# Performance work log

Hardware: AMD Instinct MI355X
Metric: run time of the kernel (lower is better)

The kernel has to match this reference:

```python
import jax, jax.numpy as jnp
import numpy as np

K = 1  # BaseSnapFunction.k default

def setup_inputs() -> dict:
    key = jax.random.key(0)
    k1, k2 = jax.random.split(key)
    B, S, D = 4, 2048, 1024
    C, N = 16, 2048          # num_codebooks, num_codes
    x = jax.random.normal(k1, (B, S, D), dtype=jnp.float32)
    codebook = jax.random.normal(k2, (C, N, D // C), dtype=jnp.float32)
    return {"x": x, "codebook": codebook}

def reference(x, codebook):
    B, S, D = x.shape
    C, N, sub = codebook.shape
    xr = x.reshape(B, S, C, sub)                      # split dim into C chunks
    # squared euclidean distance (monotone in true distance -> same argmin)
    dots = jnp.einsum('bscd,cnd->bscn', xr, codebook)  # [B,S,C,N]
    xsq = jnp.sum(xr * xr, axis=-1)                    # [B,S,C]
    cbsq = jnp.sum(codebook * codebook, axis=-1)       # [C,N]
    d2 = xsq[..., None] - 2.0 * dots + cbsq[None, None]
    idx = jnp.argmin(d2, axis=-1)                      # [B,S,C], k=1 topk of -dist
    # gather per-codebook features and concat chunks back to dim
    quant = codebook[jnp.arange(C)[None, None, :], idx]  # [B,S,C,sub]
    out = quant.reshape(B, S, D) / K
    return out
```

## Files before the change

kernel.cpp:

```cpp
#include <hip/hip_runtime.h>

constexpr int BS    = 8192;
constexpr int CCH   = 16;
constexpr int NCODE = 2048;

using s16x8 = __attribute__((ext_vector_type(8))) short;
using f32x4 = __attribute__((ext_vector_type(4))) float;


__device__ __forceinline__ unsigned short bf16_rne(float v) {
    unsigned u = __float_as_uint(v);
    return (unsigned short)((u + 0x7fffu + ((u >> 16) & 1u)) >> 16);
}
__device__ __forceinline__ void split1(float v, unsigned short& h, unsigned short& l) {
    h = bf16_rne(v);
    const float hf = __uint_as_float((unsigned)h << 16);
    l = bf16_rne(v - hf);
}
__device__ __forceinline__ void split4(float4 v, ushort4& h, ushort4& l) {
    split1(v.x, h.x, l.x); split1(v.y, h.y, l.y);
    split1(v.z, h.z, l.z); split1(v.w, h.w, l.w);
}
__device__ __forceinline__ unsigned enc_f(float s) {
    unsigned u = __float_as_uint(s);
    return (u & 0x80000000u) ? ~u : (u | 0x80000000u);
}

__device__ __forceinline__ s16x8 ldfrag(const char* buf, int row, int ke) {
    return *(const s16x8*)(buf + row * 128 + ((((ke >> 3) ^ row) & 7) * 16));
}

__device__ __forceinline__ void gload16(const void* g, void* l) {
    __builtin_amdgcn_global_load_lds(
        (const __attribute__((address_space(1))) void*)g,
        (__attribute__((address_space(3))) void*)l, 16, 0, 0);
}

__global__ void cbsq_kernel(const float* __restrict__ cb, float* __restrict__ cbsq,
                            float* __restrict__ cmax)
{
    const int g = blockIdx.x * 256 + threadIdx.x;
    const float4* cg = (const float4*)cb;
    float s = 0.f;
#pragma unroll
    for (int q = 0; q < 16; ++q) {
        float4 v = cg[(size_t)g * 16 + q];
        s = fmaf(v.x, v.x, s); s = fmaf(v.y, v.y, s);
        s = fmaf(v.z, v.z, s); s = fmaf(v.w, v.w, s);
    }
    cbsq[g] = s;
    atomicMax((unsigned*)cmax, __float_as_uint(s));
}

__global__ void presplit_cb(const float* __restrict__ cb,
                            unsigned short* __restrict__ cbh,
                            unsigned short* __restrict__ cbl)
{
    const int g = blockIdx.x * 256 + threadIdx.x;
    const float4 v = ((const float4*)cb)[g];
    ushort4 h, l; split4(v, h, l);
    ((ushort4*)cbh)[g] = h;
    ((ushort4*)cbl)[g] = l;
}

__global__ __launch_bounds__(256, 2)
void vq_fp32_fallback(const float* __restrict__ x, const float* __restrict__ cb,
                      float* __restrict__ out)
{
    __shared__ __align__(16) char smraw[65536];
    float4 (*xs)[128] = reinterpret_cast<float4(*)[128]>(smraw);
    float4 (*cs)[128] = reinterpret_cast<float4(*)[128]>(smraw + 32768);
    float  (*rs)[128] = reinterpret_cast<float(*)[128]>(smraw);
    int    (*ri)[128] = reinterpret_cast<int(*)[128]>(smraw + 8192);
    int    *bfin      = reinterpret_cast<int*>(smraw + 16384);

    const int tid = threadIdx.x, tx = tid & 15, ty = tid >> 4;
    const int c = blockIdx.y, mbase = blockIdx.x * 128;
    const float4* xg = (const float4*)x;
    const float4* cg = (const float4*)cb;
    {
        const int k4 = tid & 15, mrow0 = tid >> 4;
#pragma unroll
        for (int i = 0; i < 8; ++i) {
            const int m = i * 16 + mrow0;
            xs[k4][m] = xg[(size_t)(mbase + m) * 256 + c * 16 + k4];
        }
    }
    float best[8]; int bidx[8];
#pragma unroll
    for (int ii = 0; ii < 8; ++ii) { best[ii] = 3.4e38f; bidx[ii] = 0; }
    for (int nt = 0; nt < 16; ++nt) {
        __syncthreads();
        {
            const int k4 = tid & 15, nrow0 = tid >> 4;
#pragma unroll
            for (int i = 0; i < 8; ++i) {
                const int n = i * 16 + nrow0;
                cs[k4][n] = cg[((size_t)c * NCODE + nt * 128 + n) * 16 + k4];
            }
        }
        __syncthreads();
        float acc[8][8], csq[8];
#pragma unroll
        for (int ii = 0; ii < 8; ++ii)
#pragma unroll
            for (int jj = 0; jj < 8; ++jj) acc[ii][jj] = 0.f;
#pragma unroll
        for (int jj = 0; jj < 8; ++jj) csq[jj] = 0.f;
#pragma unroll 2
        for (int k4 = 0; k4 < 16; ++k4) {
            float4 xv[8], cv[8];
#pragma unroll
            for (int ii = 0; ii < 8; ++ii) xv[ii] = xs[k4][tx + 16 * ii];
#pragma unroll
            for (int jj = 0; jj < 8; ++jj) cv[jj] = cs[k4][ty + 16 * jj];
#pragma unroll
            for (int jj = 0; jj < 8; ++jj) {
                csq[jj] = fmaf(cv[jj].x, cv[jj].x, csq[jj]);
                csq[jj] = fmaf(cv[jj].y, cv[jj].y, csq[jj]);
                csq[jj] = fmaf(cv[jj].z, cv[jj].z, csq[jj]);
                csq[jj] = fmaf(cv[jj].w, cv[jj].w, csq[jj]);
            }
#pragma unroll
            for (int ii = 0; ii < 8; ++ii)
#pragma unroll
                for (int jj = 0; jj < 8; ++jj) {
                    acc[ii][jj] = fmaf(xv[ii].x, cv[jj].x, acc[ii][jj]);
                    acc[ii][jj] = fmaf(xv[ii].y, cv[jj].y, acc[ii][jj]);
                    acc[ii][jj] = fmaf(xv[ii].z, cv[jj].z, acc[ii][jj]);
                    acc[ii][jj] = fmaf(xv[ii].w, cv[jj].w, acc[ii][jj]);
                }
        }
#pragma unroll
        for (int jj = 0; jj < 8; ++jj) {
            const int n = nt * 128 + ty + 16 * jj;
#pragma unroll
            for (int ii = 0; ii < 8; ++ii) {
                const float s = fmaf(-2.f, acc[ii][jj], csq[jj]);
                if (s < best[ii]) { best[ii] = s; bidx[ii] = n; }
            }
        }
    }
    __syncthreads();
#pragma unroll
    for (int ii = 0; ii < 8; ++ii) {
        const int m = tx + 16 * ii;
        rs[ty][m] = best[ii]; ri[ty][m] = bidx[ii];
    }
    __syncthreads();
    if (tid < 128) {
        float b = rs[0][tid]; int bi = ri[0][tid];
#pragma unroll
        for (int j = 1; j < 16; ++j) {
            const float s = rs[j][tid]; const int i2 = ri[j][tid];
            if (s < b || (s == b && i2 < bi)) { b = s; bi = i2; }
        }
        bfin[tid] = bi;
    }
    __syncthreads();
    {
        float4* og = (float4*)out;
#pragma unroll
        for (int i = 0; i < 8; ++i) {
            const int flat = i * 256 + tid, m = flat >> 4, q = flat & 15;
            og[(size_t)(mbase + m) * 256 + c * 16 + q] =
                cg[((size_t)c * NCODE + bfin[m]) * 16 + q];
        }
    }
}

template<bool PRESPLIT>
__global__ __launch_bounds__(256, 2)
void pass1(const float* __restrict__ x, const float* __restrict__ cb,
           const unsigned short* __restrict__ cbh, const unsigned short* __restrict__ cbl,
           const float* __restrict__ cbsq, const float* __restrict__ cmax,
           float* __restrict__ out, int* __restrict__ bcnt, int* __restrict__ bwl,
           unsigned long long* __restrict__ pbest)
{
    __shared__ __align__(1024) char sm[65536];
    const int tid  = threadIdx.x;
    const int lane = tid & 63, wv = tid >> 6;
    const int l15  = lane & 15, quad = lane >> 4;
    const int c = blockIdx.y, mbase = blockIdx.x * 128;
    const float4* xg = (const float4*)x;
    const float4* cg = (const float4*)cb;
    const float cmaxs = sqrtf(*cmax);
    const int cwb = (wv & 1) * 64, tkb = (wv >> 1) * 64;

    int tdec[4], ndec[4];
    {
        char* calV = sm;
        char* calO = sm + 16384;
#pragma unroll
        for (int i = 0; i < 8; ++i) {
            const int flat = i * 256 + tid, row = flat >> 4, f4c = flat & 15;
            const int off = row * 128 + ((((f4c >> 1) ^ row) & 7) * 16) + (f4c & 1) * 8;
            const unsigned short hv = bf16_rne((float)(row & 15));
            const unsigned short ho = bf16_rne(1.0f);
            ushort4 v4 = {hv, hv, hv, hv}, o4 = {ho, ho, ho, ho};
            *(ushort4*)(calV + off) = v4;
            *(ushort4*)(calO + off) = o4;
        }
        __syncthreads();
        const int ke = quad * 8;
        const s16x8 aV = ldfrag(calV, cwb + l15, ke);
        const s16x8 aO = ldfrag(calO, cwb + l15, ke);
        const s16x8 bV = ldfrag(calV, tkb + l15, ke);
        const s16x8 bO = ldfrag(calO, tkb + l15, ke);
        f32x4 z; z[0] = z[1] = z[2] = z[3] = 0.f;
        const f32x4 at = __builtin_amdgcn_mfma_f32_16x16x32_bf16(aO, bV, z, 0, 0, 0);
        const f32x4 an = __builtin_amdgcn_mfma_f32_16x16x32_bf16(aV, bO, z, 0, 0, 0);
#pragma unroll
        for (int r = 0; r < 4; ++r) {
            tdec[r] = ((int)(at[r] + 0.5f) >> 5) & 15;
            ndec[r] = ((int)(an[r] + 0.5f) >> 5) & 15;
        }
        __syncthreads();
    }

    char* xs_hi = sm;
    char* xs_lo = sm + 16384;
    {
        float4 xf[8];
#pragma unroll
        for (int i = 0; i < 8; ++i) {
            const int flat = i * 256 + tid;
            xf[i] = xg[(size_t)(mbase + (flat >> 4)) * 256 + c * 16 + (flat & 15)];
        }
#pragma unroll
        for (int i = 0; i < 8; ++i) {
            const int flat = i * 256 + tid, row = flat >> 4, f4c = flat & 15;
            ushort4 h, l; split4(xf[i], h, l);
            const int off = row * 128 + ((((f4c >> 1) ^ row) & 7) * 16) + (f4c & 1) * 8;
            *(ushort4*)(xs_hi + off) = h;
            *(ushort4*)(xs_lo + off) = l;
        }
    }
    __syncthreads();

    s16x8 bhf[4][2], blf[4][2];
#pragma unroll
    for (int jt = 0; jt < 4; ++jt)
#pragma unroll
        for (int ks = 0; ks < 2; ++ks) {
            const int rowt = tkb + jt * 16 + l15;
            const int ke = ks * 32 + quad * 8;
            bhf[jt][ks] = ldfrag(xs_hi, rowt, ke);
            blf[jt][ks] = ldfrag(xs_lo, rowt, ke);
        }

    float4 pf[8];
    uint4  ph[4], pl[4];
    if (PRESPLIT) {
        const uint4* sh = (const uint4*)(cbh + (size_t)c * NCODE * 64);
        const uint4* sl = (const uint4*)(cbl + (size_t)c * NCODE * 64);
#pragma unroll
        for (int i = 0; i < 4; ++i) {
            const int flat = i * 256 + tid;
            ph[i] = sh[flat]; pl[i] = sl[flat];
        }
    } else {
        const float4* src = cg + (size_t)c * NCODE * 16;
#pragma unroll
        for (int i = 0; i < 8; ++i) {
            const int flat = i * 256 + tid;
            pf[i] = src[(size_t)(flat >> 4) * 16 + (flat & 15)];
        }
    }

    float s1[4][4], s2[4][4]; int i1[4][4];
#pragma unroll
    for (int jt = 0; jt < 4; ++jt)
#pragma unroll
        for (int r = 0; r < 4; ++r) { s1[jt][r] = 3.4e38f; s2[jt][r] = 3.4e38f; i1[jt][r] = 0; }

    for (int nt = 0; nt < 16; ++nt) {
        char* chi = (nt & 1) ? sm : sm + 32768;
        char* clo = chi + 16384;
        if (PRESPLIT) {
#pragma unroll
            for (int i = 0; i < 4; ++i) {
                const int flat = i * 256 + tid;
                const int row = flat >> 3, ch = flat & 7;
                const int phys = (ch ^ row) & 7;
                *(uint4*)(chi + row * 128 + phys * 16) = ph[i];
                *(uint4*)(clo + row * 128 + phys * 16) = pl[i];
            }
        } else {
#pragma unroll
            for (int i = 0; i < 8; ++i) {
                const int flat = i * 256 + tid, row = flat >> 4, f4c = flat & 15;
                ushort4 h, l; split4(pf[i], h, l);
                const int off = row * 128 + ((((f4c >> 1) ^ row) & 7) * 16) + (f4c & 1) * 8;
                *(ushort4*)(chi + off) = h;
                *(ushort4*)(clo + off) = l;
            }
        }
        __syncthreads();
        if (nt < 15) {
            if (PRESPLIT) {
                const uint4* sh = (const uint4*)(cbh + ((size_t)c * NCODE + (nt + 1) * 128) * 64);
                const uint4* sl = (const uint4*)(cbl + ((size_t)c * NCODE + (nt + 1) * 128) * 64);
#pragma unroll
                for (int i = 0; i < 4; ++i) {
                    const int flat = i * 256 + tid;
                    ph[i] = sh[flat]; pl[i] = sl[flat];
                }
            } else {
                const float4* src = cg + ((size_t)c * NCODE + (nt + 1) * 128) * 16;
#pragma unroll
                for (int i = 0; i < 8; ++i) {
                    const int flat = i * 256 + tid;
                    pf[i] = src[(size_t)(flat >> 4) * 16 + (flat & 15)];
                }
            }
        }
        const float* cbn = cbsq + c * NCODE + nt * 128;
        float csqv[4][4];
#pragma unroll
        for (int mt = 0; mt < 4; ++mt)
#pragma unroll
            for (int r = 0; r < 4; ++r)
                csqv[mt][r] = cbn[cwb + mt * 16 + ndec[r]];

#pragma unroll
        for (int mt = 0; mt < 4; ++mt) {
            f32x4 accj[4];
#pragma unroll
            for (int jt = 0; jt < 4; ++jt)
#pragma unroll
                for (int e = 0; e < 4; ++e) accj[jt][e] = 0.f;
#pragma unroll
            for (int ks = 0; ks < 2; ++ks) {
                const int ke = ks * 32 + quad * 8;
                const int rowc = cwb + mt * 16 + l15;
                const s16x8 ah = ldfrag(chi, rowc, ke);
                const s16x8 al = ldfrag(clo, rowc, ke);
#pragma unroll
                for (int jt = 0; jt < 4; ++jt) {
                    accj[jt] = __builtin_amdgcn_mfma_f32_16x16x32_bf16(ah, bhf[jt][ks], accj[jt], 0, 0, 0);
                    accj[jt] = __builtin_amdgcn_mfma_f32_16x16x32_bf16(ah, blf[jt][ks], accj[jt], 0, 0, 0);
                    accj[jt] = __builtin_amdgcn_mfma_f32_16x16x32_bf16(al, bhf[jt][ks], accj[jt], 0, 0, 0);
                }
            }
#pragma unroll
            for (int jt = 0; jt < 4; ++jt)
#pragma unroll
                for (int r = 0; r < 4; ++r) {
                    const float s = fmaf(-2.f, accj[jt][r], csqv[mt][r]);
                    const int n = nt * 128 + cwb + mt * 16 + ndec[r];
                    const bool lt = s < s1[jt][r];
                    s2[jt][r] = fminf(s2[jt][r], fmaxf(s, s1[jt][r]));
                    i1[jt][r] = lt ? n : i1[jt][r];
                    s1[jt][r] = fminf(s1[jt][r], s);
                }
        }
    }

    __syncthreads();
    float* s1a = (float*)sm;
    int*   i1a = (int*)(sm + 16384);
    float* s2a = (float*)(sm + 32768);
    float* sm_part = (float*)(sm + 49152);
    int*   bfin    = (int*)(sm + 57344);
#pragma unroll
    for (int jt = 0; jt < 4; ++jt)
#pragma unroll
        for (int r = 0; r < 4; ++r) {
            const int tok = tkb + jt * 16 + tdec[r];
            const int idx = tok * 32 + (wv & 1) * 16 + ndec[r];
            s1a[idx] = s1[jt][r]; i1a[idx] = i1[jt][r]; s2a[idx] = s2[jt][r];
        }
    {
        const float4* src = xg + (size_t)mbase * 256 + c * 16;
#pragma unroll
        for (int i = 0; i < 8; ++i) {
            const int flat = i * 256 + tid, row = flat >> 4, f4c = flat & 15;
            const float4 v = src[(size_t)row * 256 + f4c];
            sm_part[row * 16 + f4c] = v.x * v.x + v.y * v.y + v.z * v.z + v.w * v.w;
        }
    }
    __syncthreads();
    if (tid < 128) {
        float b1 = 3.4e38f, b2 = 3.4e38f; int bi = 0;
#pragma unroll 4
        for (int e = 0; e < 32; ++e) {
            const float se = s1a[tid * 32 + e];
            const int   ie = i1a[tid * 32 + e];
            const float s2e = s2a[tid * 32 + e];
            if (se < b1 || (se == b1 && ie < bi)) { b2 = fminf(b2, b1); b1 = se; bi = ie; }
            else b2 = fminf(b2, se);
            b2 = fminf(b2, s2e);
        }
        float xsq = 0.f;
#pragma unroll
        for (int q = 0; q < 16; ++q) xsq += sm_part[tid * 16 + q];
        const float eps = 3e-4f + 2e-4f * sqrtf(xsq) * cmaxs;
        bfin[tid] = bi;
        if (b2 - b1 <= 2.f * eps) {
            const int slot = atomicAdd(&bcnt[c], 1);
            bwl[c * 8192 + slot] = mbase + tid;
            pbest[c * 8192 + slot] = ~0ULL;
        }
    }
    __syncthreads();
    {
        float4* og = (float4*)out;
#pragma unroll
        for (int i = 0; i < 8; ++i) {
            const int flat = i * 256 + tid, m = flat >> 4, q = flat & 15;
            og[(size_t)(mbase + m) * 256 + c * 16 + q] =
                cg[((size_t)c * NCODE + bfin[m]) * 16 + q];
        }
    }
}

__global__ __launch_bounds__(256, 2)
void pass1_gl(const float* __restrict__ x, const float* __restrict__ cb,
              const unsigned short* __restrict__ cbh, const unsigned short* __restrict__ cbl,
              const float* __restrict__ cbsq, const float* __restrict__ cmax,
              float* __restrict__ out, int* __restrict__ bcnt, int* __restrict__ bwl,
              unsigned long long* __restrict__ pbest)
{
    __shared__ __align__(1024) char sm[65536];
    const int tid  = threadIdx.x;
    const int lane = tid & 63, wv = tid >> 6;
    const int l15  = lane & 15, quad = lane >> 4;
    const int c = blockIdx.y, mbase = blockIdx.x * 128;
    const float4* xg = (const float4*)x;
    const float4* cg = (const float4*)cb;
    const float cmaxs = sqrtf(*cmax);
    const int cwb = (wv & 1) * 64, tkb = (wv >> 1) * 64;

    char* bufA = sm;
    char* bufB = sm + 32768;

    const int lanebyte = ((lane >> 3) << 7) | ((((lane & 7) ^ (lane >> 3)) & 7) << 4);
    const char* srcH = (const char*)cbh + (size_t)c * NCODE * 128;
    const char* srcL = (const char*)cbl + (size_t)c * NCODE * 128;
    const int wchunk = wv * 4096;

    float4 xf[8];
#pragma unroll
    for (int i = 0; i < 8; ++i) {
        const int flat = i * 256 + tid;
        xf[i] = xg[(size_t)(mbase + (flat >> 4)) * 256 + c * 16 + (flat & 15)];
    }
#pragma unroll
    for (int j = 0; j < 4; ++j) {
        const int o = wchunk + j * 1024;
        gload16(srcH + o + lanebyte, bufB + o);
        gload16(srcL + o + lanebyte, bufB + 16384 + o);
    }

    int tdec[4], ndec[4];
    {
        char* calV = sm;
        char* calO = sm + 16384;
#pragma unroll
        for (int i = 0; i < 8; ++i) {
            const int flat = i * 256 + tid, row = flat >> 4, f4c = flat & 15;
            const int off = row * 128 + ((((f4c >> 1) ^ row) & 7) * 16) + (f4c & 1) * 8;
            const unsigned short hv = bf16_rne((float)(row & 15));
            const unsigned short ho = bf16_rne(1.0f);
            ushort4 v4 = {hv, hv, hv, hv}, o4 = {ho, ho, ho, ho};
            *(ushort4*)(calV + off) = v4;
            *(ushort4*)(calO + off) = o4;
        }
        __syncthreads();
        const int ke = quad * 8;
        const s16x8 aV = ldfrag(calV, cwb + l15, ke);
        const s16x8 aO = ldfrag(calO, cwb + l15, ke);
        const s16x8 bV = ldfrag(calV, tkb + l15, ke);
        const s16x8 bO = ldfrag(calO, tkb + l15, ke);
        f32x4 z; z[0] = z[1] = z[2] = z[3] = 0.f;
        const f32x4 at = __builtin_amdgcn_mfma_f32_16x16x32_bf16(aO, bV, z, 0, 0, 0);
        const f32x4 an = __builtin_amdgcn_mfma_f32_16x16x32_bf16(aV, bO, z, 0, 0, 0);
#pragma unroll
        for (int r = 0; r < 4; ++r) {
            tdec[r] = ((int)(at[r] + 0.5f) >> 5) & 15;
            ndec[r] = ((int)(an[r] + 0.5f) >> 5) & 15;
        }
        __syncthreads();
    }

    float p8[8];
#pragma unroll
    for (int i = 0; i < 8; ++i) {
        const int flat = i * 256 + tid, row = flat >> 4, f4c = flat & 15;
        ushort4 h, l; split4(xf[i], h, l);
        const int off = row * 128 + ((((f4c >> 1) ^ row) & 7) * 16) + (f4c & 1) * 8;
        *(ushort4*)(bufA + off) = h;
        *(ushort4*)(bufA + 16384 + off) = l;
        p8[i] = xf[i].x * xf[i].x + xf[i].y * xf[i].y + xf[i].z * xf[i].z + xf[i].w * xf[i].w;
    }
    __syncthreads();

    s16x8 bhf[4][2], blf[4][2];
#pragma unroll
    for (int jt = 0; jt < 4; ++jt)
#pragma unroll
        for (int ks = 0; ks < 2; ++ks) {
            const int rowt = tkb + jt * 16 + l15;
            const int ke = ks * 32 + quad * 8;
            bhf[jt][ks] = ldfrag(bufA, rowt, ke);
            blf[jt][ks] = ldfrag(bufA + 16384, rowt, ke);
        }
    __syncthreads();

    float s1[4][4], s2[4][4]; int i1[4][4];
#pragma unroll
    for (int jt = 0; jt < 4; ++jt)
#pragma unroll
        for (int r = 0; r < 4; ++r) { s1[jt][r] = 3.4e38f; s2[jt][r] = 3.4e38f; i1[jt][r] = 0; }

    for (int nt = 0; nt < 16; ++nt) {
        char* chi = (nt & 1) ? bufA : bufB;
        char* clo = chi + 16384;
        if (nt < 15) {
            char* nh = (nt & 1) ? bufB : bufA;
            const char* th = srcH + (size_t)(nt + 1) * 16384;
            const char* tl = srcL + (size_t)(nt + 1) * 16384;
#pragma unroll
            for (int j = 0; j < 4; ++j) {
                const int o = wchunk + j * 1024;
                gload16(th + o + lanebyte, nh + o);
                gload16(tl + o + lanebyte, nh + 16384 + o);
            }
        }
        const float* cbn = cbsq + c * NCODE + nt * 128;
        float csqv[4][4];
#pragma unroll
        for (int mt = 0; mt < 4; ++mt)
#pragma unroll
            for (int r = 0; r < 4; ++r)
                csqv[mt][r] = cbn[cwb + mt * 16 + ndec[r]];

#pragma unroll
        for (int mt = 0; mt < 4; ++mt) {
            f32x4 accj[4];
#pragma unroll
            for (int jt = 0; jt < 4; ++jt)
#pragma unroll
                for (int e = 0; e < 4; ++e) accj[jt][e] = 0.f;
#pragma unroll
            for (int ks = 0; ks < 2; ++ks) {
                const int ke = ks * 32 + quad * 8;
                const int rowc = cwb + mt * 16 + l15;
                const s16x8 ah = ldfrag(chi, rowc, ke);
                const s16x8 al = ldfrag(clo, rowc, ke);
#pragma unroll
                for (int jt = 0; jt < 4; ++jt) {
                    accj[jt] = __builtin_amdgcn_mfma_f32_16x16x32_bf16(ah, bhf[jt][ks], accj[jt], 0, 0, 0);
                    accj[jt] = __builtin_amdgcn_mfma_f32_16x16x32_bf16(ah, blf[jt][ks], accj[jt], 0, 0, 0);
                    accj[jt] = __builtin_amdgcn_mfma_f32_16x16x32_bf16(al, bhf[jt][ks], accj[jt], 0, 0, 0);
                }
            }
#pragma unroll
            for (int jt = 0; jt < 4; ++jt)
#pragma unroll
                for (int r = 0; r < 4; ++r) {
                    const float s = fmaf(-2.f, accj[jt][r], csqv[mt][r]);
                    const int n = nt * 128 + cwb + mt * 16 + ndec[r];
                    const bool lt = s < s1[jt][r];
                    s2[jt][r] = fminf(s2[jt][r], fmaxf(s, s1[jt][r]));
                    i1[jt][r] = lt ? n : i1[jt][r];
                    s1[jt][r] = fminf(s1[jt][r], s);
                }
        }
        __syncthreads();
    }

    float* s1a = (float*)sm;
    int*   i1a = (int*)(sm + 16896);
    float* s2a = (float*)(sm + 33792);
    float* sm_part = (float*)(sm + 50688);
    int*   bfin    = (int*)(sm + 58880);
#pragma unroll
    for (int jt = 0; jt < 4; ++jt)
#pragma unroll
        for (int r = 0; r < 4; ++r) {
            const int tok = tkb + jt * 16 + tdec[r];
            const int idx = tok * 33 + (wv & 1) * 16 + ndec[r];
            s1a[idx] = s1[jt][r]; i1a[idx] = i1[jt][r]; s2a[idx] = s2[jt][r];
        }
#pragma unroll
    for (int i = 0; i < 8; ++i) {
        const int flat = i * 256 + tid, row = flat >> 4, f4c = flat & 15;
        sm_part[row * 16 + f4c] = p8[i];
    }
    __syncthreads();
    if (tid < 128) {
        float b1 = 3.4e38f, b2 = 3.4e38f; int bi = 0;
#pragma unroll 4
        for (int e = 0; e < 32; ++e) {
            const float se = s1a[tid * 33 + e];
            const int   ie = i1a[tid * 33 + e];
            const float s2e = s2a[tid * 33 + e];
            if (se < b1 || (se == b1 && ie < bi)) { b2 = fminf(b2, b1); b1 = se; bi = ie; }
            else b2 = fminf(b2, se);
            b2 = fminf(b2, s2e);
        }
        float xsq = 0.f;
#pragma unroll
        for (int q = 0; q < 16; ++q) xsq += sm_part[tid * 16 + q];
        const float eps = 3e-4f + 2e-4f * sqrtf(xsq) * cmaxs;
        bfin[tid] = bi;
        if (b2 - b1 <= 2.f * eps) {
            const int slot = atomicAdd(&bcnt[c], 1);
            bwl[c * 8192 + slot] = mbase + tid;
            pbest[c * 8192 + slot] = ~0ULL;
        }
    }
    __syncthreads();
    {
        float4* og = (float4*)out;
#pragma unroll
        for (int i = 0; i < 8; ++i) {
            const int flat = i * 256 + tid, m = flat >> 4, q = flat & 15;
            og[(size_t)(mbase + m) * 256 + c * 16 + q] =
                cg[((size_t)c * NCODE + bfin[m]) * 16 + q];
        }
    }
}

__global__ __launch_bounds__(256, 2)
void pass2_nt(const float* __restrict__ x, const float* __restrict__ cb,
              const int* __restrict__ bcnt, const int* __restrict__ bwl,
              unsigned long long* __restrict__ pbest)
{
    __shared__ __align__(16) char smraw[65536];
    __shared__ int toks[128];
    float4 (*xs)[128] = reinterpret_cast<float4(*)[128]>(smraw);
    float4 (*cs)[128] = reinterpret_cast<float4(*)[128]>(smraw + 32768);
    float  (*rs)[128] = reinterpret_cast<float(*)[128]>(smraw);
    int    (*ri)[128] = reinterpret_cast<int(*)[128]>(smraw + 8192);

    const int c = blockIdx.y, ntb = blockIdx.x;
    const int cnt = bcnt[c];
    if (cnt == 0) return;
    const int tid = threadIdx.x, tx = tid & 15, ty = tid >> 4;
    const float4* xg = (const float4*)x;
    const float4* cg = (const float4*)cb;

    {
        const int k4 = tid & 15, nrow0 = tid >> 4;
#pragma unroll
        for (int i = 0; i < 8; ++i) {
            const int n = i * 16 + nrow0;
            cs[k4][n] = cg[((size_t)c * NCODE + ntb * 128 + n) * 16 + k4];
        }
    }

    for (int g0 = 0; g0 < cnt; g0 += 128) {
        __syncthreads();
        if (tid < 128) {
            const int e = g0 + tid;
            toks[tid] = bwl[c * 8192 + (e < cnt ? e : g0)];
        }
        __syncthreads();
        {
            const int k4 = tid & 15, mrow0 = tid >> 4;
#pragma unroll
            for (int i = 0; i < 8; ++i) {
                const int m = i * 16 + mrow0;
                xs[k4][m] = xg[(size_t)toks[m] * 256 + c * 16 + k4];
            }
        }
        __syncthreads();
        float acc[8][8], csq[8];
#pragma unroll
        for (int ii = 0; ii < 8; ++ii)
#pragma unroll
            for (int jj = 0; jj < 8; ++jj) acc[ii][jj] = 0.f;
#pragma unroll
        for (int jj = 0; jj < 8; ++jj) csq[jj] = 0.f;
#pragma unroll 2
        for (int k4 = 0; k4 < 16; ++k4) {
            float4 xv[8], cv[8];
#pragma unroll
            for (int ii = 0; ii < 8; ++ii) xv[ii] = xs[k4][tx + 16 * ii];
#pragma unroll
            for (int jj = 0; jj < 8; ++jj) cv[jj] = cs[k4][ty + 16 * jj];
#pragma unroll
            for (int jj = 0; jj < 8; ++jj) {
                csq[jj] = fmaf(cv[jj].x, cv[jj].x, csq[jj]);
                csq[jj] = fmaf(cv[jj].y, cv[jj].y, csq[jj]);
                csq[jj] = fmaf(cv[jj].z, cv[jj].z, csq[jj]);
                csq[jj] = fmaf(cv[jj].w, cv[jj].w, csq[jj]);
            }
#pragma unroll
            for (int ii = 0; ii < 8; ++ii)
#pragma unroll
                for (int jj = 0; jj < 8; ++jj) {
                    acc[ii][jj] = fmaf(xv[ii].x, cv[jj].x, acc[ii][jj]);
                    acc[ii][jj] = fmaf(xv[ii].y, cv[jj].y, acc[ii][jj]);
                    acc[ii][jj] = fmaf(xv[ii].z, cv[jj].z, acc[ii][jj]);
                    acc[ii][jj] = fmaf(xv[ii].w, cv[jj].w, acc[ii][jj]);
                }
        }
        float best[8]; int bidx[8];
#pragma unroll
        for (int ii = 0; ii < 8; ++ii) { best[ii] = 3.4e38f; bidx[ii] = 0; }
#pragma unroll
        for (int jj = 0; jj < 8; ++jj) {
            const int n = ntb * 128 + ty + 16 * jj;
#pragma unroll
            for (int ii = 0; ii < 8; ++ii) {
                const float s = fmaf(-2.f, acc[ii][jj], csq[jj]);
                if (s < best[ii]) { best[ii] = s; bidx[ii] = n; }
            }
        }
        __syncthreads();
#pragma unroll
        for (int ii = 0; ii < 8; ++ii) {
            const int m = tx + 16 * ii;
            rs[ty][m] = best[ii]; ri[ty][m] = bidx[ii];
        }
        __syncthreads();
        if (tid < 128 && g0 + tid < cnt) {
            float b = rs[0][tid]; int bi = ri[0][tid];
#pragma unroll
            for (int j = 1; j < 16; ++j) {
                const float s = rs[j][tid]; const int i2 = ri[j][tid];
                if (s < b || (s == b && i2 < bi)) { b = s; bi = i2; }
            }
            const unsigned long long pk =
                ((unsigned long long)enc_f(b) << 32) | (unsigned)bi;
            atomicMin(&pbest[c * 8192 + g0 + tid], pk);
        }
    }
}

__global__ void pass3(const float* __restrict__ cb, float* __restrict__ out,
                      const int* __restrict__ bcnt, const int* __restrict__ bwl,
                      const unsigned long long* __restrict__ pbest)
{
    const int c = blockIdx.y;
    const int cnt = bcnt[c];
    const float4* cg = (const float4*)cb;
    float4* og = (float4*)out;
    const int q = threadIdx.x & 15;
    for (int e = blockIdx.x * 16 + (threadIdx.x >> 4); e < cnt; e += 64 * 16) {
        const int tok = bwl[c * 8192 + e];
        const unsigned n = (unsigned)(pbest[c * 8192 + e] & 0xFFFFFFFFull);
        og[(size_t)tok * 256 + c * 16 + q] = cg[((size_t)c * NCODE + n) * 16 + q];
    }
}

extern "C" void kernel_launch(void* const* d_in, const int* in_sizes, int n_in,
                              void* d_out, int out_size, void* d_ws, size_t ws_size,
                              hipStream_t stream)
{
    const float* x  = (const float*)d_in[0];
    const float* cb = (const float*)d_in[1];
    float* out      = (float*)d_out;

    if (ws_size < (size_t)(2u << 20)) {
        dim3 grid(BS / 128, CCH);
        vq_fp32_fallback<<<grid, 256, 0, stream>>>(x, cb, out);
        return;
    }
    char* ws = (char*)d_ws;
    float* cbsq = (float*)ws;
    float* cmax = (float*)(ws + 131072);
    int*   bcnt = (int*)(ws + 131076);
    int*   bwl  = (int*)(ws + 131328);
    unsigned long long* pbest = (unsigned long long*)(ws + 655616);
    unsigned short* cbh = (unsigned short*)(ws + (2u << 20));
    unsigned short* cbl = (unsigned short*)(ws + (6u << 20));

    hipMemsetAsync(ws + 131072, 0, 68, stream);
    cbsq_kernel<<<CCH * NCODE / 256, 256, 0, stream>>>(cb, cbsq, cmax);
    if (ws_size >= (size_t)(10u << 20)) {
        presplit_cb<<<2048, 256, 0, stream>>>(cb, cbh, cbl);
        pass1_gl<<<dim3(BS / 128, CCH), 256, 0, stream>>>(x, cb, cbh, cbl, cbsq, cmax, out, bcnt, bwl, pbest);
    } else {
        pass1<false><<<dim3(BS / 128, CCH), 256, 0, stream>>>(x, cb, nullptr, nullptr, cbsq, cmax, out, bcnt, bwl, pbest);
    }
    pass2_nt<<<dim3(16, CCH), 256, 0, stream>>>(x, cb, bcnt, bwl, pbest);
    pass3<<<dim3(64, CCH), 256, 0, stream>>>(cb, out, bcnt, bwl, pbest);
}
```

Baseline: 229.7 us.

## Shrink pass1 LDS to 48KB with 64-code tiles for three blocks per CU

The pass1 kernel's shared-memory footprint drops from 64KB to 48KB. The x tile stays resident while two 64-code codebook buffers alternate, one of them aliasing the x area after its fragments are loaded into registers. The code loop now runs 32 iterations of 64 codes instead of 16 of 128, and launch bounds ask for 3 blocks per CU. The final top-2 reduction switches from LDS scatter plus a serial scan to register merges and wave shuffles, and the calibration MFMA is built from register constants instead of LDS. The cost is twice as many barriers and a tighter register budget per thread, which could cause spills.

```diff
diff --git a/kernel.cpp b/kernel.cpp
--- a/kernel.cpp
+++ b/kernel.cpp
@@ -34,6 +34,12 @@
     __builtin_amdgcn_global_load_lds(
         (const __attribute__((address_space(1))) void*)g,
         (__attribute__((address_space(3))) void*)l, 16, 0, 0);
+}
+
+__device__ __forceinline__ void merge2(float& b1, int& bi, float& b2,
+                                       float ob1, int obi, float ob2) {
+    b2 = fminf(fminf(b2, ob2), fmaxf(b1, ob1));
+    if (ob1 < b1 || (ob1 == b1 && obi < bi)) { b1 = ob1; bi = obi; }
 }
 
 __global__ void cbsq_kernel(const float* __restrict__ cb, float* __restrict__ cbsq,
@@ -415,14 +421,14 @@
     }
 }
 
-__global__ __launch_bounds__(256, 2)
+__global__ __launch_bounds__(256, 3)
 void pass1_gl(const float* __restrict__ x, const float* __restrict__ cb,
               const unsigned short* __restrict__ cbh, const unsigned short* __restrict__ cbl,
               const float* __restrict__ cbsq, const float* __restrict__ cmax,
               float* __restrict__ out, int* __restrict__ bcnt, int* __restrict__ bwl,
               unsigned long long* __restrict__ pbest)
 {
-    __shared__ __align__(1024) char sm[65536];
+    __shared__ __align__(1024) char sm[49152];
     const int tid  = threadIdx.x;
     const int lane = tid & 63, wv = tid >> 6;
     const int l15  = lane & 15, quad = lane >> 4;
@@ -430,15 +436,18 @@
     const float4* xg = (const float4*)x;
     const float4* cg = (const float4*)cb;
     const float cmaxs = sqrtf(*cmax);
-    const int cwb = (wv & 1) * 64, tkb = (wv >> 1) * 64;
-
-    char* bufA = sm;
-    char* bufB = sm + 32768;
+    const int cwb = (wv & 1) * 32;
+    const int tkb = (wv >> 1) * 64;
+
+    char* xs_hi = sm;
+    char* xs_lo = sm + 16384;
+    char* buf0  = sm + 32768;
+    char* buf1  = sm;
 
     const int lanebyte = ((lane >> 3) << 7) | ((((lane & 7) ^ (lane >> 3)) & 7) << 4);
     const char* srcH = (const char*)cbh + (size_t)c * NCODE * 128;
     const char* srcL = (const char*)cbl + (size_t)c * NCODE * 128;
-    const int wchunk = wv * 4096;
+    const int wchunk = wv * 2048;
 
     float4 xf[8];
 #pragma unroll
@@ -447,41 +456,27 @@
         xf[i] = xg[(size_t)(mbase + (flat >> 4)) * 256 + c * 16 + (flat & 15)];
     }
 #pragma unroll
-    for (int j = 0; j < 4; ++j) {
+    for (int j = 0; j < 2; ++j) {
         const int o = wchunk + j * 1024;
-        gload16(srcH + o + lanebyte, bufB + o);
-        gload16(srcL + o + lanebyte, bufB + 16384 + o);
+        gload16(srcH + o + lanebyte, buf0 + o);
+        gload16(srcL + o + lanebyte, buf0 + 8192 + o);
     }
 
     int tdec[4], ndec[4];
     {
-        char* calV = sm;
-        char* calO = sm + 16384;
-#pragma unroll
-        for (int i = 0; i < 8; ++i) {
-            const int flat = i * 256 + tid, row = flat >> 4, f4c = flat & 15;
-            const int off = row * 128 + ((((f4c >> 1) ^ row) & 7) * 16) + (f4c & 1) * 8;
-            const unsigned short hv = bf16_rne((float)(row & 15));
-            const unsigned short ho = bf16_rne(1.0f);
-            ushort4 v4 = {hv, hv, hv, hv}, o4 = {ho, ho, ho, ho};
-            *(ushort4*)(calV + off) = v4;
-            *(ushort4*)(calO + off) = o4;
-        }
-        __syncthreads();
-        const int ke = quad * 8;
-        const s16x8 aV = ldfrag(calV, cwb + l15, ke);
-        const s16x8 aO = ldfrag(calO, cwb + l15, ke);
-        const s16x8 bV = ldfrag(calV, tkb + l15, ke);
-        const s16x8 bO = ldfrag(calO, tkb + l15, ke);
+        const short one = (short)bf16_rne(1.0f);
+        const short val = (short)bf16_rne((float)l15);
+        s16x8 aV, aO;
+#pragma unroll
+        for (int e = 0; e < 8; ++e) { aV[e] = val; aO[e] = one; }
         f32x4 z; z[0] = z[1] = z[2] = z[3] = 0.f;
-        const f32x4 at = __builtin_amdgcn_mfma_f32_16x16x32_bf16(aO, bV, z, 0, 0, 0);
-        const f32x4 an = __builtin_amdgcn_mfma_f32_16x16x32_bf16(aV, bO, z, 0, 0, 0);
+        const f32x4 at = __builtin_amdgcn_mfma_f32_16x16x32_bf16(aO, aV, z, 0, 0, 0);
+        const f32x4 an = __builtin_amdgcn_mfma_f32_16x16x32_bf16(aV, aO, z, 0, 0, 0);
 #pragma unroll
         for (int r = 0; r < 4; ++r) {
             tdec[r] = ((int)(at[r] + 0.5f) >> 5) & 15;
             ndec[r] = ((int)(an[r] + 0.5f) >> 5) & 15;
         }
-        __syncthreads();
     }
 
     float p8[8];
@@ -490,8 +485,8 @@
         const int flat = i * 256 + tid, row = flat >> 4, f4c = flat & 15;
         ushort4 h, l; split4(xf[i], h, l);
         const int off = row * 128 + ((((f4c >> 1) ^ row) & 7) * 16) + (f4c & 1) * 8;
-        *(ushort4*)(bufA + off) = h;
-        *(ushort4*)(bufA + 16384 + off) = l;
+        *(ushort4*)(xs_hi + off) = h;
+        *(ushort4*)(xs_lo + off) = l;
         p8[i] = xf[i].x * xf[i].x + xf[i].y * xf[i].y + xf[i].z * xf[i].z + xf[i].w * xf[i].w;
     }
     __syncthreads();
@@ -503,8 +498,8 @@
         for (int ks = 0; ks < 2; ++ks) {
             const int rowt = tkb + jt * 16 + l15;
             const int ke = ks * 32 + quad * 8;
-            bhf[jt][ks] = ldfrag(bufA, rowt, ke);
-            blf[jt][ks] = ldfrag(bufA + 16384, rowt, ke);
+            bhf[jt][ks] = ldfrag(xs_hi, rowt, ke);
+            blf[jt][ks] = ldfrag(xs_lo, rowt, ke);
         }
     __syncthreads();
 
@@ -514,30 +509,30 @@
 #pragma unroll
         for (int r = 0; r < 4; ++r) { s1[jt][r] = 3.4e38f; s2[jt][r] = 3.4e38f; i1[jt][r] = 0; }
 
-    for (int nt = 0; nt < 16; ++nt) {
-        char* chi = (nt & 1) ? bufA : bufB;
-        char* clo = chi + 16384;
-        if (nt < 15) {
-            char* nh = (nt & 1) ? bufB : bufA;
-            const char* th = srcH + (size_t)(nt + 1) * 16384;
-            const char* tl = srcL + (size_t)(nt + 1) * 16384;
-#pragma unroll
-            for (int j = 0; j < 4; ++j) {
+    for (int nt = 0; nt < 32; ++nt) {
+        char* chi = (nt & 1) ? buf1 : buf0;
+        char* clo = chi + 8192;
+        if (nt < 31) {
+            char* nh = (nt & 1) ? buf0 : buf1;
+            const char* th = srcH + (size_t)(nt + 1) * 8192;
+            const char* tl = srcL + (size_t)(nt + 1) * 8192;
+#pragma unroll
+            for (int j = 0; j < 2; ++j) {
                 const int o = wchunk + j * 1024;
                 gload16(th + o + lanebyte, nh + o);
-                gload16(tl + o + lanebyte, nh + 16384 + o);
-            }
-        }
-        const float* cbn = cbsq + c * NCODE + nt * 128;
-        float csqv[4][4];
-#pragma unroll
-        for (int mt = 0; mt < 4; ++mt)
+                gload16(tl + o + lanebyte, nh + 8192 + o);
+            }
+        }
+        const float* cbn = cbsq + c * NCODE + nt * 64;
+        float csqv[2][4];
+#pragma unroll
+        for (int mt = 0; mt < 2; ++mt)
 #pragma unroll
             for (int r = 0; r < 4; ++r)
                 csqv[mt][r] = cbn[cwb + mt * 16 + ndec[r]];
 
 #pragma unroll
-        for (int mt = 0; mt < 4; ++mt) {
+        for (int mt = 0; mt < 2; ++mt) {
             f32x4 accj[4];
 #pragma unroll
             for (int jt = 0; jt < 4; ++jt)
@@ -561,7 +556,7 @@
 #pragma unroll
                 for (int r = 0; r < 4; ++r) {
                     const float s = fmaf(-2.f, accj[jt][r], csqv[mt][r]);
-                    const int n = nt * 128 + cwb + mt * 16 + ndec[r];
+                    const int n = nt * 64 + cwb + mt * 16 + ndec[r];
                     const bool lt = s < s1[jt][r];
                     s2[jt][r] = fminf(s2[jt][r], fmaxf(s, s1[jt][r]));
                     i1[jt][r] = lt ? n : i1[jt][r];
@@ -571,39 +566,44 @@
         __syncthreads();
     }
 
-    float* s1a = (float*)sm;
-    int*   i1a = (int*)(sm + 16896);
-    float* s2a = (float*)(sm + 33792);
-    float* sm_part = (float*)(sm + 50688);
-    int*   bfin    = (int*)(sm + 58880);
-#pragma unroll
-    for (int jt = 0; jt < 4; ++jt)
-#pragma unroll
-        for (int r = 0; r < 4; ++r) {
-            const int tok = tkb + jt * 16 + tdec[r];
-            const int idx = tok * 33 + (wv & 1) * 16 + ndec[r];
-            s1a[idx] = s1[jt][r]; i1a[idx] = i1[jt][r]; s2a[idx] = s2[jt][r];
-        }
+    float* s1h = (float*)(sm + 16384);
+    int*   i1h = (int*)  (sm + 17408);
+    float* s2h = (float*)(sm + 18432);
+    float* xsq_l = (float*)(sm + 19456);
+    int*   bfin  = (int*)  (sm + 19968);
+
+#pragma unroll
+    for (int jt = 0; jt < 4; ++jt) {
+        float b1 = s1[jt][0], b2 = s2[jt][0]; int bi = i1[jt][0];
+#pragma unroll
+        for (int r = 1; r < 4; ++r)
+            merge2(b1, bi, b2, s1[jt][r], i1[jt][r], s2[jt][r]);
+#pragma unroll
+        for (int m = 16; m <= 32; m <<= 1) {
+            const float ob1 = __shfl_xor(b1, m);
+            const int   obi = __shfl_xor(bi, m);
+            const float ob2 = __shfl_xor(b2, m);
+            merge2(b1, bi, b2, ob1, obi, ob2);
+        }
+        if (quad == 0) {
+            const int tok = tkb + jt * 16 + tdec[0];
+            s1h[tok * 2 + (wv & 1)] = b1;
+            i1h[tok * 2 + (wv & 1)] = bi;
+            s2h[tok * 2 + (wv & 1)] = b2;
+        }
+    }
 #pragma unroll
     for (int i = 0; i < 8; ++i) {
-        const int flat = i * 256 + tid, row = flat >> 4, f4c = flat & 15;
-        sm_part[row * 16 + f4c] = p8[i];
+        float v = p8[i];
+        v += __shfl_xor(v, 1); v += __shfl_xor(v, 2);
+        v += __shfl_xor(v, 4); v += __shfl_xor(v, 8);
+        if (l15 == 0) xsq_l[i * 16 + (tid >> 4)] = v;
     }
     __syncthreads();
     if (tid < 128) {
-        float b1 = 3.4e38f, b2 = 3.4e38f; int bi = 0;
-#pragma unroll 4
-        for (int e = 0; e < 32; ++e) {
-            const float se = s1a[tid * 33 + e];
-            const int   ie = i1a[tid * 33 + e];
-            const float s2e = s2a[tid * 33 + e];
-            if (se < b1 || (se == b1 && ie < bi)) { b2 = fminf(b2, b1); b1 = se; bi = ie; }
-            else b2 = fminf(b2, se);
-            b2 = fminf(b2, s2e);
-        }
-        float xsq = 0.f;
-#pragma unroll
-        for (int q = 0; q < 16; ++q) xsq += sm_part[tid * 16 + q];
+        float b1 = s1h[tid * 2], b2 = s2h[tid * 2]; int bi = i1h[tid * 2];
+        merge2(b1, bi, b2, s1h[tid * 2 + 1], i1h[tid * 2 + 1], s2h[tid * 2 + 1]);
+        const float xsq = xsq_l[tid];
         const float eps = 3e-4f + 2e-4f * sqrtf(xsq) * cmaxs;
         bfin[tid] = bi;
         if (b2 - b1 <= 2.f * eps) {
```

After: 298.4 us. 1.3x slower.
